# Kernel tuning notes

Hardware: AMD Instinct MI355X
Metric: run time of the kernel (lower is better)

Reference implementation:

```python
import jax, jax.numpy as jnp
import numpy as np

NUM_HEADS = 16
HEAD_DIM = 64
ROT_DIM = HEAD_DIM // 2  # RotaryEmbedding(dim=head_dim/2) rotates first 32 dims only
THETA = 10000.0


def _rope(x):
    # x: [b, h, l, d]; interleaved (lucidrains) rotary on first ROT_DIM dims.
    L = x.shape[-2]
    inv_freq = 1.0 / (THETA ** (jnp.arange(0, ROT_DIM, 2, dtype=jnp.float32) / ROT_DIM))  # [ROT_DIM/2]
    ang = jnp.arange(L, dtype=jnp.float32)[:, None] * inv_freq[None, :]  # [l, ROT_DIM/2]
    ang = jnp.repeat(ang, 2, axis=-1)  # [l, ROT_DIM] (each freq repeated for the pair)
    cos, sin = jnp.cos(ang), jnp.sin(ang)
    x_rot, x_pass = x[..., :ROT_DIM], x[..., ROT_DIM:]
    x1 = x_rot[..., 0::2]
    x2 = x_rot[..., 1::2]
    rot_half = jnp.stack([-x2, x1], axis=-1).reshape(x_rot.shape)  # rotate_half, interleaved
    x_rot = x_rot * cos + rot_half * sin
    return jnp.concatenate([x_rot, x_pass], axis=-1)


def setup_inputs() -> dict:
    key = jax.random.key(0)
    ks = jax.random.split(key, 7)
    B, L, E = 2, 2048, 1024
    s = 1.0 / np.sqrt(E)
    return {
        "query": jax.random.normal(ks[0], (B, L, E), jnp.float32),
        "key": jax.random.normal(ks[1], (B, L, E), jnp.float32),
        "value": jax.random.normal(ks[2], (B, L, E), jnp.float32),
        "Wq": jax.random.normal(ks[3], (E, E), jnp.float32) * s,
        "Wk": jax.random.normal(ks[4], (E, E), jnp.float32) * s,
        "Wv": jax.random.normal(ks[5], (E, E), jnp.float32) * s,
        "Wo": jax.random.normal(ks[6], (E, E), jnp.float32) * s,
        "bo": jnp.zeros((E,), jnp.float32),
    }


def reference(query, key, value, Wq, Wk, Wv, Wo, bo):
    B, L, E = query.shape
    H, D = NUM_HEADS, HEAD_DIM
    scaling = D ** (-0.5)

    def split_heads(x):
        return x.reshape(B, L, H, D).transpose(0, 2, 1, 3)  # b h l d

    q = split_heads(query @ Wq.T)
    k = split_heads(key @ Wk.T)
    v = split_heads(value @ Wv.T)
    q = _rope(q)
    k = _rope(k)
    # NOTE: source divides by scaling (multiplies by sqrt(D)) -- faithful to original.
    attn_weight = jnp.einsum('bhid,bhjd->bhij', q, k) / scaling
    # NOTE: softmax over dim=-2 (query axis), as in the original code.
    attn_weight = jax.nn.softmax(attn_weight, axis=-2)
    attn = jnp.einsum('bhij,bhjd->bhid', attn_weight, v)
    attn = attn.transpose(0, 2, 1, 3).reshape(B, L, E)
    out = attn @ Wo.T + bo
    return out, attn_weight
```

## Files before the change

kernel.cpp:

```cpp
#include <hip/hip_runtime.h>
#include <cmath>

typedef __bf16 bf16;
typedef __attribute__((ext_vector_type(4))) __bf16 bf16x4;
typedef __attribute__((ext_vector_type(8))) __bf16 bf16x8;
typedef __attribute__((ext_vector_type(4))) float f32x4;

#define MFMA16(a, b, c) __builtin_amdgcn_mfma_f32_16x16x32_bf16((a), (b), (c), 0, 0, 0)
#define SETPRIO1 __builtin_amdgcn_s_setprio(1)
#define SETPRIO0 __builtin_amdgcn_s_setprio(0)
#define WAITV_BAR(N) asm volatile("s_waitcnt vmcnt(" #N ")\n\ts_barrier" ::: "memory")
#define WAITL_BAR    asm volatile("s_waitcnt lgkmcnt(0)\n\ts_barrier" ::: "memory")

#define LOG2E 1.4426950408889634f

static __device__ __forceinline__ void gload16(const bf16* g, bf16* l)
{
  __builtin_amdgcn_global_load_lds((const __attribute__((address_space(1))) void*)g,
                                   (__attribute__((address_space(3))) void*)l, 16, 0, 0);
}

static __device__ __forceinline__ void split4(const float4 v, bf16x4& h, bf16x4& l)
{
  h[0] = (bf16)v.x; l[0] = (bf16)(v.x - (float)h[0]);
  h[1] = (bf16)v.y; l[1] = (bf16)(v.y - (float)h[1]);
  h[2] = (bf16)v.z; l[2] = (bf16)(v.z - (float)h[2]);
  h[3] = (bf16)v.w; l[3] = (bf16)(v.w - (float)h[3]);
}

__global__ __launch_bounds__(256) void conv_kernel(
    const float* __restrict__ query, const float* __restrict__ key, const float* __restrict__ value,
    const float* __restrict__ Wq, const float* __restrict__ Wk, const float* __restrict__ Wv,
    const float* __restrict__ Wo,
    bf16* __restrict__ qh, bf16* __restrict__ ql, bf16* __restrict__ kh, bf16* __restrict__ kl,
    bf16* __restrict__ wqh, bf16* __restrict__ wql, bf16* __restrict__ wkh, bf16* __restrict__ wkl,
    bf16* __restrict__ vb, bf16* __restrict__ wvb, bf16* __restrict__ wob)
{
  const int i = blockIdx.x * 256 + threadIdx.x;
  const float* src;
  bf16 *dh, *dl;
  int e;
  if (i < 1048576)      { src = query; dh = qh; dl = ql; e = i; }
  else if (i < 2097152) { src = key;   dh = kh; dl = kl; e = i - 1048576; }
  else if (i < 3145728) { src = value; dh = vb; dl = nullptr; e = i - 2097152; }
  else {
    const int w = i - 3145728;
    const int which = w >> 18;
    e = w & 262143;
    src = (which == 0) ? Wq : (which == 1) ? Wk : (which == 2) ? Wv : Wo;
    dh  = (which == 0) ? wqh : (which == 1) ? wkh : (which == 2) ? wvb : wob;
    dl  = (which == 0) ? wql : (which == 1) ? wkl : nullptr;
  }
  const float4 v = ((const float4*)src)[e];
  bf16x4 h, l;
  split4(v, h, l);
  *(bf16x4*)(dh + (size_t)e * 4) = h;
  if (dl) *(bf16x4*)(dl + (size_t)e * 4) = l;
}

__global__ __launch_bounds__(256) void projqk_kernel(
    const bf16* __restrict__ qh, const bf16* __restrict__ ql,
    const bf16* __restrict__ kh, const bf16* __restrict__ kl,
    const bf16* __restrict__ wqh, const bf16* __restrict__ wql,
    const bf16* __restrict__ wkh, const bf16* __restrict__ wkl,
    bf16* __restrict__ Qh_g, bf16* __restrict__ Ql_g,
    bf16* __restrict__ Kh_g, bf16* __restrict__ Kl_g)
{
  const int which = blockIdx.y;
  const bf16* ta[4];
  ta[0] = which ? kh : qh;   ta[1] = which ? kl : ql;
  ta[2] = which ? wkh : wqh; ta[3] = which ? wkl : wql;
  bf16* oh = which ? Kh_g : Qh_g;
  bf16* ol = which ? Kl_g : Ql_g;
  const float oscale = which ? 8.0f * LOG2E : 1.0f;

  __shared__ __align__(16) bf16 sm[2][4][4096];
  const int tid = threadIdx.x, lane = tid & 63, w = tid >> 6;
  const int wm = w >> 1, wn = w & 1;
  const int fr = lane & 15, fg = lane >> 4;
  const int bm = blockIdx.x >> 3, bn = blockIdx.x & 7;
  const int rb[4] = {bm * 128, bm * 128, bn * 128, bn * 128};
  const int lrow = lane >> 2, lcol = (lane & 3) * 8;

  auto stage = [&](int buf, int kt) {
#pragma unroll
    for (int tl = 0; tl < 4; ++tl)
#pragma unroll
      for (int q = 0; q < 2; ++q) {
        const int r = (q * 4 + w) * 16 + lrow;
        gload16(ta[tl] + (size_t)(rb[tl] + r) * 1024 + kt * 32 + lcol,
                &sm[buf][tl][(q * 4 + w) * 512]);
      }
  };

  f32x4 acc[4][4] = {};
  stage(0, 0);
  for (int kt = 0; kt < 32; ++kt) {
    const int cur = kt & 1;
    if (kt < 31) { stage(cur ^ 1, kt + 1); WAITV_BAR(8); }
    else         { WAITV_BAR(0); }
    bf16x8 afh[4], afl[4], bfh[4], bfl[4];
#pragma unroll
    for (int m = 0; m < 4; ++m) {
      afh[m] = *(bf16x8*)&sm[cur][0][(wm * 64 + m * 16 + fr) * 32 + fg * 8];
      afl[m] = *(bf16x8*)&sm[cur][1][(wm * 64 + m * 16 + fr) * 32 + fg * 8];
    }
#pragma unroll
    for (int n = 0; n < 4; ++n) {
      bfh[n] = *(bf16x8*)&sm[cur][2][(wn * 64 + n * 16 + fr) * 32 + fg * 8];
      bfl[n] = *(bf16x8*)&sm[cur][3][(wn * 64 + n * 16 + fr) * 32 + fg * 8];
    }
    SETPRIO1;
#pragma unroll
    for (int m = 0; m < 4; ++m)
#pragma unroll
      for (int n = 0; n < 4; ++n) {
        acc[m][n] = MFMA16(afh[m], bfh[n], acc[m][n]);
        acc[m][n] = MFMA16(afh[m], bfl[n], acc[m][n]);
        acc[m][n] = MFMA16(afl[m], bfh[n], acc[m][n]);
      }
    SETPRIO0;
    WAITL_BAR;
  }
#pragma unroll
  for (int n = 0; n < 4; ++n) {
    const int d = n * 16 + fr;
    const bool rot = (n < 2);
    const float invf = rot ? exp2f((float)(d >> 1) * (-0.83048202372184059f)) : 0.0f;
    const int odd = d & 1;
    const int col = bn * 128 + wn * 64 + n * 16 + fr;
#pragma unroll
    for (int m = 0; m < 4; ++m)
#pragma unroll
      for (int r4 = 0; r4 < 4; ++r4) {
        const int row = bm * 128 + wm * 64 + m * 16 + fg * 4 + r4;
        float x = acc[m][n][r4];
        const float p = __shfl_xor(x, 1);
        if (rot) {
          float sn, cs;
          sincosf((float)(row & 2047) * invf, &sn, &cs);
          x = odd ? x * cs + p * sn : x * cs - p * sn;
        }
        x *= oscale;
        const bf16 hv = (bf16)x;
        oh[(size_t)row * 1024 + col] = hv;
        ol[(size_t)row * 1024 + col] = (bf16)(x - (float)hv);
      }
  }
}

__global__ __launch_bounds__(256) void projv_kernel(const bf16* __restrict__ vb,
                                                    const bf16* __restrict__ wvb,
                                                    bf16* __restrict__ Vt_g)
{
  __shared__ __align__(16) bf16 sm[2][2][4096];
  const int tid = threadIdx.x, lane = tid & 63, w = tid >> 6;
  const int wm = w >> 1, wn = w & 1;
  const int fr = lane & 15, fg = lane >> 4;
  const int bm = blockIdx.x >> 3, bn = blockIdx.x & 7;
  const int lrow = lane >> 2, lcol = (lane & 3) * 8;

  auto stage = [&](int buf, int kt) {
#pragma unroll
    for (int q = 0; q < 2; ++q) {
      const int r = (q * 4 + w) * 16 + lrow;
      gload16(vb  + (size_t)(bm * 128 + r) * 1024 + kt * 32 + lcol, &sm[buf][0][(q * 4 + w) * 512]);
      gload16(wvb + (size_t)(bn * 128 + r) * 1024 + kt * 32 + lcol, &sm[buf][1][(q * 4 + w) * 512]);
    }
  };

  f32x4 acc[4][4] = {};
  stage(0, 0);
  for (int kt = 0; kt < 32; ++kt) {
    const int cur = kt & 1;
    if (kt < 31) { stage(cur ^ 1, kt + 1); WAITV_BAR(4); }
    else         { WAITV_BAR(0); }
    bf16x8 af[4], bf[4];
#pragma unroll
    for (int m = 0; m < 4; ++m) af[m] = *(bf16x8*)&sm[cur][0][(wm * 64 + m * 16 + fr) * 32 + fg * 8];
#pragma unroll
    for (int n = 0; n < 4; ++n) bf[n] = *(bf16x8*)&sm[cur][1][(wn * 64 + n * 16 + fr) * 32 + fg * 8];
    SETPRIO1;
#pragma unroll
    for (int m = 0; m < 4; ++m)
#pragma unroll
      for (int n = 0; n < 4; ++n) acc[m][n] = MFMA16(af[m], bf[n], acc[m][n]);
    SETPRIO0;
    WAITL_BAR;
  }
#pragma unroll
  for (int m = 0; m < 4; ++m) {
    const int row0 = bm * 128 + wm * 64 + m * 16 + fg * 4;
    const int b = row0 >> 11, l0 = row0 & 2047;
#pragma unroll
    for (int n = 0; n < 4; ++n) {
      const int col = bn * 128 + wn * 64 + n * 16 + fr;
      const int h = col >> 6, d = col & 63;
      bf16x4 pk;
#pragma unroll
      for (int j = 0; j < 4; ++j) pk[j] = (bf16)acc[m][n][j];
      *(bf16x4*)(Vt_g + ((size_t)((b * 16 + h) * 64 + d)) * 2048 + l0) = pk;
    }
  }
}

__global__ __launch_bounds__(256) void out_kernel(const bf16* __restrict__ attnb,
                                                  const bf16* __restrict__ wob,
                                                  const float* __restrict__ bo,
                                                  float* __restrict__ out)
{
  __shared__ __align__(16) bf16 sm[2][2][4096];
  const int tid = threadIdx.x, lane = tid & 63, w = tid >> 6;
  const int wm = w >> 1, wn = w & 1;
  const int fr = lane & 15, fg = lane >> 4;
  const int bm = blockIdx.x >> 3, bn = blockIdx.x & 7;
  const int lrow = lane >> 2, lcol = (lane & 3) * 8;

  auto stage = [&](int buf, int kt) {
#pragma unroll
    for (int q = 0; q < 2; ++q) {
      const int r = (q * 4 + w) * 16 + lrow;
      gload16(attnb + (size_t)(bm * 128 + r) * 1024 + kt * 32 + lcol, &sm[buf][0][(q * 4 + w) * 512]);
      gload16(wob   + (size_t)(bn * 128 + r) * 1024 + kt * 32 + lcol, &sm[buf][1][(q * 4 + w) * 512]);
    }
  };

  f32x4 acc[4][4] = {};
  stage(0, 0);
  for (int kt = 0; kt < 32; ++kt) {
    const int cur = kt & 1;
    if (kt < 31) { stage(cur ^ 1, kt + 1); WAITV_BAR(4); }
    else         { WAITV_BAR(0); }
    bf16x8 af[4], bf[4];
#pragma unroll
    for (int m = 0; m < 4; ++m) af[m] = *(bf16x8*)&sm[cur][0][(wm * 64 + m * 16 + fr) * 32 + fg * 8];
#pragma unroll
    for (int n = 0; n < 4; ++n) bf[n] = *(bf16x8*)&sm[cur][1][(wn * 64 + n * 16 + fr) * 32 + fg * 8];
    SETPRIO1;
#pragma unroll
    for (int m = 0; m < 4; ++m)
#pragma unroll
      for (int n = 0; n < 4; ++n) acc[m][n] = MFMA16(af[m], bf[n], acc[m][n]);
    SETPRIO0;
    WAITL_BAR;
  }
#pragma unroll
  for (int m = 0; m < 4; ++m)
#pragma unroll
    for (int n = 0; n < 4; ++n) {
      const int col = bn * 128 + wn * 64 + n * 16 + fr;
      const float bv = bo[col];
#pragma unroll
      for (int r4 = 0; r4 < 4; ++r4) {
        const int row = bm * 128 + wm * 64 + m * 16 + fg * 4 + r4;
        out[(size_t)row * 1024 + col] = acc[m][n][r4] + bv;
      }
    }
}

__global__ __launch_bounds__(512) void stats_kernel(const bf16* __restrict__ Qh_g, const bf16* __restrict__ Ql_g,
                                                    const bf16* __restrict__ Kh_g, const bf16* __restrict__ Kl_g,
                                                    float* __restrict__ colmax, float* __restrict__ csuminv)
{
  __shared__ __align__(16) bf16 smh[2][8192], sml[2][8192];
  const int swz = (blockIdx.x & 7) * 64 + (blockIdx.x >> 3);
  const int bh = swz >> 4, jb = swz & 15;
  const int b = bh >> 4, h = bh & 15;
  const int t = threadIdx.x, lane = t & 63, w = t >> 6;
  const int fr = lane & 15, fg = lane >> 4;
  const int lr = lane >> 3, lc = lane & 7;

  auto stageQ = [&](int buf, int it) {
#pragma unroll
    for (int q = 0; q < 2; ++q) {
      const int r = (q * 8 + w) * 8 + lr;
      const size_t g = (size_t)(b * 2048 + it * 128 + r) * 1024 + h * 64 + ((lc ^ (r & 7)) * 8);
      gload16(Qh_g + g, &smh[buf][(q * 8 + w) * 512]);
      gload16(Ql_g + g, &sml[buf][(q * 8 + w) * 512]);
    }
  };

#pragma unroll
  for (int q = 0; q < 2; ++q) {
    const int r = (q * 8 + w) * 8 + lr;
    const size_t g = (size_t)(b * 2048 + jb * 128 + r) * 1024 + h * 64 + ((lc ^ (r & 7)) * 8);
    gload16(Kh_g + g, &smh[1][(q * 8 + w) * 512]);
    gload16(Kl_g + g, &sml[1][(q * 8 + w) * 512]);
  }
  stageQ(0, 0);
  WAITV_BAR(4);
  bf16x8 kfh[2], kfl[2];
#pragma unroll
  for (int ks = 0; ks < 2; ++ks) {
    const int rr = w * 16 + fr;
    const int cc = (ks * 32 + fg * 8) ^ ((rr & 7) << 3);
    kfh[ks] = *(bf16x8*)&smh[1][rr * 64 + cc];
    kfl[ks] = *(bf16x8*)&sml[1][rr * 64 + cc];
  }
  WAITL_BAR;

  float rm[4] = {-1e30f, -1e30f, -1e30f, -1e30f};
  float rs[4] = {0.f, 0.f, 0.f, 0.f};
  for (int it = 0; it < 16; ++it) {
    const int cur = it & 1;
    if (it < 15) { stageQ(cur ^ 1, it + 1); WAITV_BAR(4); }
    else         { WAITV_BAR(0); }
    f32x4 acc[8] = {};
    SETPRIO1;
#pragma unroll
    for (int ks = 0; ks < 2; ++ks)
#pragma unroll
      for (int n = 0; n < 8; ++n) {
        const int rr = n * 16 + fr;
        const int cc = (ks * 32 + fg * 8) ^ ((rr & 7) << 3);
        const bf16x8 qf = *(bf16x8*)&smh[cur][rr * 64 + cc];
        const bf16x8 lf = *(bf16x8*)&sml[cur][rr * 64 + cc];
        acc[n] = MFMA16(kfh[ks], qf, acc[n]);
        acc[n] = MFMA16(kfh[ks], lf, acc[n]);
        acc[n] = MFMA16(kfl[ks], qf, acc[n]);
      }
    SETPRIO0;
    float tm[4];
#pragma unroll
    for (int r4 = 0; r4 < 4; ++r4) {
      float m = acc[0][r4];
#pragma unroll
      for (int n = 1; n < 8; ++n) m = fmaxf(m, acc[n][r4]);
      tm[r4] = m;
    }
#pragma unroll
    for (int off = 1; off < 16; off <<= 1)
#pragma unroll
      for (int r4 = 0; r4 < 4; ++r4) tm[r4] = fmaxf(tm[r4], __shfl_xor(tm[r4], off));
#pragma unroll
    for (int r4 = 0; r4 < 4; ++r4) {
      const float mn = fmaxf(rm[r4], tm[r4]);
      float ts = 0.f;
#pragma unroll
      for (int n = 0; n < 8; ++n) ts += exp2f(acc[n][r4] - mn);
#pragma unroll
      for (int off = 1; off < 16; off <<= 1) ts += __shfl_xor(ts, off);
      rs[r4] = rs[r4] * exp2f(rm[r4] - mn) + ts;
      rm[r4] = mn;
    }
    WAITL_BAR;
  }
  if (fr == 0) {
#pragma unroll
    for (int r4 = 0; r4 < 4; ++r4) {
      const int j = jb * 128 + w * 16 + fg * 4 + r4;
      colmax[bh * 2048 + j] = rm[r4];
      csuminv[bh * 2048 + j] = 1.0f / rs[r4];
    }
  }
}

__global__ __launch_bounds__(256) void attn_kernel(const bf16* __restrict__ Qh_g, const bf16* __restrict__ Ql_g,
                                                   const bf16* __restrict__ Kh_g, const bf16* __restrict__ Kl_g,
                                                   const bf16* __restrict__ Vt_g,
                                                   const float* __restrict__ colmax, const float* __restrict__ csuminv,
                                                   float* __restrict__ P, bf16* __restrict__ attnb)
{
  __shared__ __align__(16) unsigned char smem[46080];
  bf16(*Kh)[72] = (bf16(*)[72])smem;
  bf16(*Kl)[72] = (bf16(*)[72])(smem + 9216);
  bf16(*Vt)[72] = (bf16(*)[72])(smem + 18432);
  bf16(*Pb)[72] = (bf16(*)[72])(smem + 27648);
  bf16(*Qh)[72] = (bf16(*)[72])smem;
  bf16(*Ql)[72] = (bf16(*)[72])(smem + 18432);

  const int swz = (blockIdx.x & 7) * 64 + (blockIdx.x >> 3);
  const int bh = swz >> 4, ib = swz & 15;
  const int b = bh >> 4, h = bh & 15;
  const int t = threadIdx.x, lane = t & 63, w = t >> 6;
  const int fr = lane & 15, fg = lane >> 4;

#pragma unroll
  for (int q = 0; q < 4; ++q) {
    const int u = q * 256 + t, r = u >> 3, c8 = (u & 7) * 8;
    const size_t g = (size_t)(b * 2048 + ib * 128 + r) * 1024 + h * 64 + c8;
    *(bf16x8*)&Qh[r][c8] = *(const bf16x8*)(Qh_g + g);
    *(bf16x8*)&Ql[r][c8] = *(const bf16x8*)(Ql_g + g);
  }
  WAITL_BAR;
  bf16x8 qfh[2][2], qfl[2][2];
#pragma unroll
  for (int mf = 0; mf < 2; ++mf)
#pragma unroll
    for (int ks = 0; ks < 2; ++ks) {
      qfh[mf][ks] = *(bf16x8*)&Qh[w * 32 + mf * 16 + fr][ks * 32 + fg * 8];
      qfl[mf][ks] = *(bf16x8*)&Ql[w * 32 + mf * 16 + fr][ks * 32 + fg * 8];
    }

  bf16x8 rKh[2], rKl[2], rV[2];
  auto loadT = [&](int jt1) {
#pragma unroll
    for (int q = 0; q < 2; ++q) {
      const int u = q * 256 + t, r = u >> 3, c8 = (u & 7) * 8;
      const size_t g = (size_t)(b * 2048 + jt1 * 64 + r) * 1024 + h * 64 + c8;
      rKh[q] = *(const bf16x8*)(Kh_g + g);
      rKl[q] = *(const bf16x8*)(Kl_g + g);
      rV[q]  = *(const bf16x8*)(Vt_g + (size_t)(bh * 64 + r) * 2048 + jt1 * 64 + c8);
    }
  };
  auto writeT = [&]() {
#pragma unroll
    for (int q = 0; q < 2; ++q) {
      const int u = q * 256 + t, r = u >> 3, c8 = (u & 7) * 8;
      *(bf16x8*)&Kh[r][c8] = rKh[q];
      *(bf16x8*)&Kl[r][c8] = rKl[q];
      *(bf16x8*)&Vt[r][c8] = rV[q];
    }
  };

  loadT(0);
  WAITL_BAR;
  writeT();
  WAITL_BAR;

  f32x4 oacc[2][4] = {};
  for (int jt = 0; jt < 32; ++jt) {
    if (jt < 31) loadT(jt + 1);
    f32x4 s[2][4] = {};
    SETPRIO1;
#pragma unroll
    for (int ks = 0; ks < 2; ++ks)
#pragma unroll
      for (int nj = 0; nj < 4; ++nj) {
        const bf16x8 khf = *(bf16x8*)&Kh[nj * 16 + fr][ks * 32 + fg * 8];
        const bf16x8 klf = *(bf16x8*)&Kl[nj * 16 + fr][ks * 32 + fg * 8];
#pragma unroll
        for (int mf = 0; mf < 2; ++mf) {
          s[mf][nj] = MFMA16(khf, qfh[mf][ks], s[mf][nj]);
          s[mf][nj] = MFMA16(klf, qfh[mf][ks], s[mf][nj]);
          s[mf][nj] = MFMA16(khf, qfl[mf][ks], s[mf][nj]);
        }
      }
    SETPRIO0;
#pragma unroll
    for (int nj = 0; nj < 4; ++nj) {
      const int jb4 = jt * 64 + nj * 16 + fg * 4;
      const f32x4 cmv = *(const f32x4*)(colmax + bh * 2048 + jb4);
      const f32x4 rcv = *(const f32x4*)(csuminv + bh * 2048 + jb4);
#pragma unroll
      for (int mf = 0; mf < 2; ++mf) {
        const int ig = ib * 128 + w * 32 + mf * 16 + fr;
        f32x4 pv;
        pv[0] = exp2f(s[mf][nj][0] - cmv[0]) * rcv[0];
        pv[1] = exp2f(s[mf][nj][1] - cmv[1]) * rcv[1];
        pv[2] = exp2f(s[mf][nj][2] - cmv[2]) * rcv[2];
        pv[3] = exp2f(s[mf][nj][3] - cmv[3]) * rcv[3];
        *(f32x4*)(P + (size_t)(bh * 2048 + ig) * 2048 + jb4) = pv;
        bf16x4 pb4;
        pb4[0] = (bf16)pv[0]; pb4[1] = (bf16)pv[1]; pb4[2] = (bf16)pv[2]; pb4[3] = (bf16)pv[3];
        *(bf16x4*)&Pb[w * 32 + mf * 16 + fr][nj * 16 + fg * 4] = pb4;
      }
    }
    WAITL_BAR;
    SETPRIO1;
#pragma unroll
    for (int ks = 0; ks < 2; ++ks) {
      bf16x8 pa[2];
#pragma unroll
      for (int mf = 0; mf < 2; ++mf) pa[mf] = *(bf16x8*)&Pb[w * 32 + mf * 16 + fr][ks * 32 + fg * 8];
#pragma unroll
      for (int nd = 0; nd < 4; ++nd) {
        const bf16x8 vbf = *(bf16x8*)&Vt[nd * 16 + fr][ks * 32 + fg * 8];
#pragma unroll
        for (int mf = 0; mf < 2; ++mf) oacc[mf][nd] = MFMA16(vbf, pa[mf], oacc[mf][nd]);
      }
    }
    SETPRIO0;
    WAITL_BAR;
    if (jt < 31) { writeT(); WAITL_BAR; }
  }
#pragma unroll
  for (int mf = 0; mf < 2; ++mf) {
    const int ig = ib * 128 + w * 32 + mf * 16 + fr;
#pragma unroll
    for (int nd = 0; nd < 4; ++nd) {
      bf16x4 o4;
#pragma unroll
      for (int r4 = 0; r4 < 4; ++r4) o4[r4] = (bf16)oacc[mf][nd][r4];
      *(bf16x4*)(attnb + (size_t)(b * 2048 + ig) * 1024 + h * 64 + nd * 16 + fg * 4) = o4;
    }
  }
}

extern "C" void kernel_launch(void* const* d_in, const int* in_sizes, int n_in,
                              void* d_out, int out_size, void* d_ws, size_t ws_size,
                              hipStream_t stream)
{
  const float* query = (const float*)d_in[0];
  const float* key   = (const float*)d_in[1];
  const float* value = (const float*)d_in[2];
  const float* Wq    = (const float*)d_in[3];
  const float* Wk    = (const float*)d_in[4];
  const float* Wv    = (const float*)d_in[5];
  const float* Wo    = (const float*)d_in[6];
  const float* bo    = (const float*)d_in[7];

  float* out = (float*)d_out;
  float* P   = out + 4194304;

  bf16* qh  = (bf16*)(P + 0);
  bf16* ql  = (bf16*)(P + 2097152);
  bf16* kh  = (bf16*)(P + 4194304);
  bf16* kl  = (bf16*)(P + 6291456);
  bf16* wqh = (bf16*)(P + 8388608);
  bf16* wql = (bf16*)(P + 8912896);
  bf16* wkh = (bf16*)(P + 9437184);
  bf16* wkl = (bf16*)(P + 9961472);
  bf16* vb  = (bf16*)(P + 10485760);
  bf16* wvb = (bf16*)(P + 12582912);

  float* ws   = (float*)d_ws;
  bf16* Qh_g  = (bf16*)(ws + 0);
  bf16* Ql_g  = (bf16*)(ws + 2097152);
  bf16* Kh_g  = (bf16*)(ws + 4194304);
  bf16* Kl_g  = (bf16*)(ws + 6291456);
  bf16* Vt_g  = (bf16*)(ws + 8388608);
  bf16* attnb = (bf16*)(ws + 10485760);
  bf16* wob   = (bf16*)(ws + 12582912);
  float* cmax = ws + 13107200;
  float* csui = ws + 13172736;

  conv_kernel<<<16384, 256, 0, stream>>>(query, key, value, Wq, Wk, Wv, Wo,
                                         qh, ql, kh, kl, wqh, wql, wkh, wkl, vb, wvb, wob);
  projqk_kernel<<<dim3(256, 2), 256, 0, stream>>>(qh, ql, kh, kl, wqh, wql, wkh, wkl,
                                                  Qh_g, Ql_g, Kh_g, Kl_g);
  projv_kernel<<<256, 256, 0, stream>>>(vb, wvb, Vt_g);
  stats_kernel<<<512, 512, 0, stream>>>(Qh_g, Ql_g, Kh_g, Kl_g, cmax, csui);
  attn_kernel<<<512, 256, 0, stream>>>(Qh_g, Ql_g, Kh_g, Kl_g, Vt_g, cmax, csui, P, attnb);
  out_kernel<<<256, 256, 0, stream>>>(attnb, wob, bo, out);
}
```

Measured before the change: 406.0 us.

## Halve attention query tile to 64 rows, double grid, use native exp2

Shrinks the attn_kernel query tile from 128 to 64 rows per block (16 per wave), doubling the grid to 1024 blocks and cutting LDS use from 45KB to 36KB. The aim is more resident blocks and better latency hiding for the bandwidth-heavy P write. The trade-off is that K/V tiles are reloaded twice as often and each K fragment feeds fewer MFMAs. It also swaps exp2f for the __builtin_amdgcn_exp2f intrinsic in both the stats and attention kernels.

```diff
diff --git a/kernel.cpp b/kernel.cpp
--- a/kernel.cpp
+++ b/kernel.cpp
@@ -9,6 +9,7 @@
 #define MFMA16(a, b, c) __builtin_amdgcn_mfma_f32_16x16x32_bf16((a), (b), (c), 0, 0, 0)
 #define SETPRIO1 __builtin_amdgcn_s_setprio(1)
 #define SETPRIO0 __builtin_amdgcn_s_setprio(0)
+#define EXP2(x) __builtin_amdgcn_exp2f(x)
 #define WAITV_BAR(N) asm volatile("s_waitcnt vmcnt(" #N ")\n\ts_barrier" ::: "memory")
 #define WAITL_BAR    asm volatile("s_waitcnt lgkmcnt(0)\n\ts_barrier" ::: "memory")
 
@@ -337,10 +338,10 @@
       const float mn = fmaxf(rm[r4], tm[r4]);
       float ts = 0.f;
 #pragma unroll
-      for (int n = 0; n < 8; ++n) ts += exp2f(acc[n][r4] - mn);
+      for (int n = 0; n < 8; ++n) ts += EXP2(acc[n][r4] - mn);
 #pragma unroll
       for (int off = 1; off < 16; off <<= 1) ts += __shfl_xor(ts, off);
-      rs[r4] = rs[r4] * exp2f(rm[r4] - mn) + ts;
+      rs[r4] = rs[r4] * EXP2(rm[r4] - mn) + ts;
       rm[r4] = mn;
     }
     WAITL_BAR;
@@ -361,36 +362,34 @@
                                                    const float* __restrict__ colmax, const float* __restrict__ csuminv,
                                                    float* __restrict__ P, bf16* __restrict__ attnb)
 {
-  __shared__ __align__(16) unsigned char smem[46080];
+  __shared__ __align__(16) unsigned char smem[36864];
   bf16(*Kh)[72] = (bf16(*)[72])smem;
   bf16(*Kl)[72] = (bf16(*)[72])(smem + 9216);
   bf16(*Vt)[72] = (bf16(*)[72])(smem + 18432);
   bf16(*Pb)[72] = (bf16(*)[72])(smem + 27648);
   bf16(*Qh)[72] = (bf16(*)[72])smem;
-  bf16(*Ql)[72] = (bf16(*)[72])(smem + 18432);
-
-  const int swz = (blockIdx.x & 7) * 64 + (blockIdx.x >> 3);
-  const int bh = swz >> 4, ib = swz & 15;
+  bf16(*Ql)[72] = (bf16(*)[72])(smem + 9216);
+
+  const int swz = (blockIdx.x & 7) * 128 + (blockIdx.x >> 3);
+  const int bh = swz >> 5, ib = swz & 31;
   const int b = bh >> 4, h = bh & 15;
   const int t = threadIdx.x, lane = t & 63, w = t >> 6;
   const int fr = lane & 15, fg = lane >> 4;
 
 #pragma unroll
-  for (int q = 0; q < 4; ++q) {
+  for (int q = 0; q < 2; ++q) {
     const int u = q * 256 + t, r = u >> 3, c8 = (u & 7) * 8;
-    const size_t g = (size_t)(b * 2048 + ib * 128 + r) * 1024 + h * 64 + c8;
+    const size_t g = (size_t)(b * 2048 + ib * 64 + r) * 1024 + h * 64 + c8;
     *(bf16x8*)&Qh[r][c8] = *(const bf16x8*)(Qh_g + g);
     *(bf16x8*)&Ql[r][c8] = *(const bf16x8*)(Ql_g + g);
   }
   WAITL_BAR;
-  bf16x8 qfh[2][2], qfl[2][2];
-#pragma unroll
-  for (int mf = 0; mf < 2; ++mf)
-#pragma unroll
-    for (int ks = 0; ks < 2; ++ks) {
-      qfh[mf][ks] = *(bf16x8*)&Qh[w * 32 + mf * 16 + fr][ks * 32 + fg * 8];
-      qfl[mf][ks] = *(bf16x8*)&Ql[w * 32 + mf * 16 + fr][ks * 32 + fg * 8];
-    }
+  bf16x8 qfh[2], qfl[2];
+#pragma unroll
+  for (int ks = 0; ks < 2; ++ks) {
+    qfh[ks] = *(bf16x8*)&Qh[w * 16 + fr][ks * 32 + fg * 8];
+    qfl[ks] = *(bf16x8*)&Ql[w * 16 + fr][ks * 32 + fg * 8];
+  }
 
   bf16x8 rKh[2], rKl[2], rV[2];
   auto loadT = [&](int jt1) {
@@ -418,10 +417,10 @@
   writeT();
   WAITL_BAR;
 
-  f32x4 oacc[2][4] = {};
+  f32x4 oacc[4] = {};
   for (int jt = 0; jt < 32; ++jt) {
     if (jt < 31) loadT(jt + 1);
-    f32x4 s[2][4] = {};
+    f32x4 s[4] = {};
     SETPRIO1;
 #pragma unroll
     for (int ks = 0; ks < 2; ++ks)
@@ -429,59 +428,51 @@
       for (int nj = 0; nj < 4; ++nj) {
         const bf16x8 khf = *(bf16x8*)&Kh[nj * 16 + fr][ks * 32 + fg * 8];
         const bf16x8 klf = *(bf16x8*)&Kl[nj * 16 + fr][ks * 32 + fg * 8];
-#pragma unroll
-        for (int mf = 0; mf < 2; ++mf) {
-          s[mf][nj] = MFMA16(khf, qfh[mf][ks], s[mf][nj]);
-          s[mf][nj] = MFMA16(klf, qfh[mf][ks], s[mf][nj]);
-          s[mf][nj] = MFMA16(khf, qfl[mf][ks], s[mf][nj]);
-        }
+        s[nj] = MFMA16(khf, qfh[ks], s[nj]);
+        s[nj] = MFMA16(klf, qfh[ks], s[nj]);
+        s[nj] = MFMA16(khf, qfl[ks], s[nj]);
       }
     SETPRIO0;
-#pragma unroll
-    for (int nj = 0; nj < 4; ++nj) {
-      const int jb4 = jt * 64 + nj * 16 + fg * 4;
-      const f32x4 cmv = *(const f32x4*)(colmax + bh * 2048 + jb4);
-      const f32x4 rcv = *(const f32x4*)(csuminv + bh * 2048 + jb4);
-#pragma unroll
-      for (int mf = 0; mf < 2; ++mf) {
-        const int ig = ib * 128 + w * 32 + mf * 16 + fr;
+    {
+      const int ig = ib * 64 + w * 16 + fr;
+#pragma unroll
+      for (int nj = 0; nj < 4; ++nj) {
+        const int jb4 = jt * 64 + nj * 16 + fg * 4;
+        const f32x4 cmv = *(const f32x4*)(colmax + bh * 2048 + jb4);
+        const f32x4 rcv = *(const f32x4*)(csuminv + bh * 2048 + jb4);
         f32x4 pv;
-        pv[0] = exp2f(s[mf][nj][0] - cmv[0]) * rcv[0];
-        pv[1] = exp2f(s[mf][nj][1] - cmv[1]) * rcv[1];
-        pv[2] = exp2f(s[mf][nj][2] - cmv[2]) * rcv[2];
-        pv[3] = exp2f(s[mf][nj][3] - cmv[3]) * rcv[3];
+        pv[0] = EXP2(s[nj][0] - cmv[0]) * rcv[0];
+        pv[1] = EXP2(s[nj][1] - cmv[1]) * rcv[1];
+        pv[2] = EXP2(s[nj][2] - cmv[2]) * rcv[2];
+        pv[3] = EXP2(s[nj][3] - cmv[3]) * rcv[3];
         *(f32x4*)(P + (size_t)(bh * 2048 + ig) * 2048 + jb4) = pv;
         bf16x4 pb4;
         pb4[0] = (bf16)pv[0]; pb4[1] = (bf16)pv[1]; pb4[2] = (bf16)pv[2]; pb4[3] = (bf16)pv[3];
-        *(bf16x4*)&Pb[w * 32 + mf * 16 + fr][nj * 16 + fg * 4] = pb4;
+        *(bf16x4*)&Pb[w * 16 + fr][nj * 16 + fg * 4] = pb4;
       }
     }
     WAITL_BAR;
     SETPRIO1;
 #pragma unroll
     for (int ks = 0; ks < 2; ++ks) {
-      bf16x8 pa[2];
-#pragma unroll
-      for (int mf = 0; mf < 2; ++mf) pa[mf] = *(bf16x8*)&Pb[w * 32 + mf * 16 + fr][ks * 32 + fg * 8];
+      const bf16x8 pa = *(bf16x8*)&Pb[w * 16 + fr][ks * 32 + fg * 8];
 #pragma unroll
       for (int nd = 0; nd < 4; ++nd) {
         const bf16x8 vbf = *(bf16x8*)&Vt[nd * 16 + fr][ks * 32 + fg * 8];
-#pragma unroll
-        for (int mf = 0; mf < 2; ++mf) oacc[mf][nd] = MFMA16(vbf, pa[mf], oacc[mf][nd]);
+        oacc[nd] = MFMA16(vbf, pa, oacc[nd]);
       }
     }
     SETPRIO0;
     WAITL_BAR;
     if (jt < 31) { writeT(); WAITL_BAR; }
   }
-#pragma unroll
-  for (int mf = 0; mf < 2; ++mf) {
-    const int ig = ib * 128 + w * 32 + mf * 16 + fr;
+  {
+    const int ig = ib * 64 + w * 16 + fr;
 #pragma unroll
     for (int nd = 0; nd < 4; ++nd) {
       bf16x4 o4;
 #pragma unroll
-      for (int r4 = 0; r4 < 4; ++r4) o4[r4] = (bf16)oacc[mf][nd][r4];
+      for (int r4 = 0; r4 < 4; ++r4) o4[r4] = (bf16)oacc[nd][r4];
       *(bf16x4*)(attnb + (size_t)(b * 2048 + ig) * 1024 + h * 64 + nd * 16 + fg * 4) = o4;
     }
   }
@@ -531,6 +522,6 @@
                                                   Qh_g, Ql_g, Kh_g, Kl_g);
   projv_kernel<<<256, 256, 0, stream>>>(vb, wvb, Vt_g);
   stats_kernel<<<512, 512, 0, stream>>>(Qh_g, Ql_g, Kh_g, Kl_g, cmax, csui);
-  attn_kernel<<<512, 256, 0, stream>>>(Qh_g, Ql_g, Kh_g, Kl_g, Vt_g, cmax, csui, P, attnb);
+  attn_kernel<<<1024, 256, 0, stream>>>(Qh_g, Ql_g, Kh_g, Kl_g, Vt_g, cmax, csui, P, attnb);
   out_kernel<<<256, 256, 0, stream>>>(attnb, wob, bo, out);
 }
```

Measured after the change: 434.2 us. 7.0% more time.
